# Kernel tuning notes

Hardware: AMD Instinct MI355X
Metric: run time of the kernel (lower is better)

The kernel has to match this reference:

```python
import jax, jax.numpy as jnp
import numpy as np

EPS = 1e-5
NUM_HEAD = 8
HEAD_DIM = 64
SCALE = HEAD_DIM ** -0.5


def setup_inputs() -> dict:
    key = jax.random.key(0)
    ks = jax.random.split(key, 3)
    b, n, dim = 4, 2048, 512
    inner = NUM_HEAD * HEAD_DIM  # 512
    x = jax.random.normal(ks[0], (b, n, dim), dtype=jnp.float32)
    ln_w = jnp.ones((dim,), jnp.float32)
    ln_b = jnp.zeros((dim,), jnp.float32)
    qkv_w = jax.random.normal(ks[1], (3 * inner, dim), jnp.float32) * (dim ** -0.5)
    qkv_b = jnp.zeros((3 * inner,), jnp.float32)
    out_w = jax.random.normal(ks[2], (dim, inner), jnp.float32) * (inner ** -0.5)
    out_b = jnp.zeros((dim,), jnp.float32)
    return {"x": x, "ln_w": ln_w, "ln_b": ln_b, "qkv_w": qkv_w,
            "qkv_b": qkv_b, "out_w": out_w, "out_b": out_b}


def reference(x, ln_w, ln_b, qkv_w, qkv_b, out_w, out_b):
    b, n, dim = x.shape
    # Pre-norm LayerNorm
    mu = jnp.mean(x, axis=-1, keepdims=True)
    var = jnp.mean(jnp.square(x - mu), axis=-1, keepdims=True)
    xn = (x - mu) * jax.lax.rsqrt(var + EPS) * ln_w + ln_b
    # QKV projection (torch Linear: y = x @ W.T + b)
    qkv = xn @ qkv_w.T + qkv_b  # [b, n, 3*inner]
    q, k, v = jnp.split(qkv, 3, axis=-1)
    def heads(t):  # [b, n, inner] -> [b, h, n, d]
        return t.reshape(b, n, NUM_HEAD, HEAD_DIM).transpose(0, 2, 1, 3)
    q, k, v = heads(q), heads(k), heads(v)
    # Naive full attention (materializes [b, h, n, n])
    dots = jnp.einsum('bhqd,bhkd->bhqk', q, k) * SCALE
    attn = jax.nn.softmax(dots, axis=-1)
    o = jnp.einsum('bhqk,bhkd->bhqd', attn, v)
    o = o.transpose(0, 2, 1, 3).reshape(b, n, NUM_HEAD * HEAD_DIM)
    return o @ out_w.T + out_b
```

## Files before the change

kernel.cpp:

```cpp
#include <hip/hip_runtime.h>

typedef __attribute__((ext_vector_type(8))) short bf16x8;
typedef __attribute__((ext_vector_type(4))) float floatx4;
typedef __attribute__((ext_vector_type(16))) float floatx16;
typedef __attribute__((ext_vector_type(4))) unsigned int uintx4;

#define B_    4
#define N_    2048
#define DIM_  512
#define NH_   8
#define HD_   64
#define SCALE_ 0.125f
#define SL2E_ (0.125f * 1.44269504f)

__device__ __forceinline__ unsigned short f32_to_bf16(float f) {
    return (unsigned short)((__float_as_uint(f) + 0x8000u) >> 16);
}

__device__ __forceinline__ float bf16_to_f32(unsigned short u) {
    return __uint_as_float(((unsigned int)u) << 16);
}

__device__ __forceinline__ floatx4 mfma16(bf16x8 a, bf16x8 b, floatx4 c) {
    return __builtin_amdgcn_mfma_f32_16x16x32_bf16(a, b, c, 0, 0, 0);
}

__device__ __forceinline__ floatx16 mfma32(bf16x8 a, bf16x8 b, floatx16 c) {
    return __builtin_amdgcn_mfma_f32_32x32x16_bf16(a, b, c, 0, 0, 0);
}

__device__ __forceinline__ floatx4 fzero4() {
    floatx4 z = {0.f, 0.f, 0.f, 0.f};
    return z;
}

__device__ __forceinline__ floatx16 fzero16() {
    floatx16 z;
#pragma unroll
    for (int i = 0; i < 16; i++) z[i] = 0.f;
    return z;
}

__device__ __forceinline__ unsigned int cvt_pk_bf16(float lo, float hi) {
    unsigned int r;
    asm("v_cvt_pk_bf16_f32 %0, %1, %2" : "=v"(r) : "v"(lo), "v"(hi));
    return r;
}

__device__ __forceinline__ void async16(const unsigned short* g, unsigned short* l) {
    __builtin_amdgcn_global_load_lds((const __attribute__((address_space(1))) void*)g,
                                     (__attribute__((address_space(3))) void*)l,
                                     16, 0, 0);
}

__global__ __launch_bounds__(256) void ln_kernel(const float* __restrict__ x,
                                                 const float* __restrict__ w,
                                                 const float* __restrict__ b,
                                                 unsigned short* __restrict__ xn) {
    int wv = threadIdx.x >> 6;
    int lane = threadIdx.x & 63;
    int row = blockIdx.x * 4 + wv;
    const float4* xr = (const float4*)(x + (size_t)row * DIM_);
    float4 v0 = xr[lane * 2];
    float4 v1 = xr[lane * 2 + 1];
    float s  = (v0.x + v0.y + v0.z + v0.w) + (v1.x + v1.y + v1.z + v1.w);
    float sq = v0.x*v0.x + v0.y*v0.y + v0.z*v0.z + v0.w*v0.w +
               v1.x*v1.x + v1.y*v1.y + v1.z*v1.z + v1.w*v1.w;
#pragma unroll
    for (int off = 1; off < 64; off <<= 1) {
        s  += __shfl_xor(s, off, 64);
        sq += __shfl_xor(sq, off, 64);
    }
    float mu   = s * (1.f / DIM_);
    float var  = sq * (1.f / DIM_) - mu * mu;
    float rstd = rsqrtf(var + 1e-5f);
    float4 w0 = ((const float4*)w)[lane * 2];
    float4 w1 = ((const float4*)w)[lane * 2 + 1];
    float4 b0 = ((const float4*)b)[lane * 2];
    float4 b1 = ((const float4*)b)[lane * 2 + 1];
    float y[8];
    y[0] = (v0.x - mu) * rstd * w0.x + b0.x;
    y[1] = (v0.y - mu) * rstd * w0.y + b0.y;
    y[2] = (v0.z - mu) * rstd * w0.z + b0.z;
    y[3] = (v0.w - mu) * rstd * w0.w + b0.w;
    y[4] = (v1.x - mu) * rstd * w1.x + b1.x;
    y[5] = (v1.y - mu) * rstd * w1.y + b1.y;
    y[6] = (v1.z - mu) * rstd * w1.z + b1.z;
    y[7] = (v1.w - mu) * rstd * w1.w + b1.w;
    uint4 pk;
    pk.x = (unsigned int)f32_to_bf16(y[0]) | ((unsigned int)f32_to_bf16(y[1]) << 16);
    pk.y = (unsigned int)f32_to_bf16(y[2]) | ((unsigned int)f32_to_bf16(y[3]) << 16);
    pk.z = (unsigned int)f32_to_bf16(y[4]) | ((unsigned int)f32_to_bf16(y[5]) << 16);
    pk.w = (unsigned int)f32_to_bf16(y[6]) | ((unsigned int)f32_to_bf16(y[7]) << 16);
    ((uint4*)(xn + (size_t)row * DIM_))[lane] = pk;
}

__global__ __launch_bounds__(256) void cvt_kernel(const float* __restrict__ srcA, int na,
                                                  const float* __restrict__ srcB, int nb,
                                                  unsigned short* __restrict__ dstA,
                                                  unsigned short* __restrict__ dstB) {
    int idx = blockIdx.x * 256 + threadIdx.x;
    if (idx < na)            dstA[idx] = f32_to_bf16(srcA[idx]);
    else if (idx < na + nb)  dstB[idx - na] = f32_to_bf16(srcB[idx - na]);
}

#define GEMM_CORE512(A_, B_ptr, am0, bn0)                                           \
    __shared__ unsigned short Alds[2][128][32];                                     \
    __shared__ unsigned short Blds[2][128][32];                                     \
    int tid = threadIdx.x, lane = tid & 63, wid = tid >> 6;                         \
    int l15 = lane & 15, quad = lane >> 4;                                          \
    int wmloc = (wid >> 1) * 32, wnloc = (wid & 1) * 64;                            \
    int sr = lane >> 2;                                                             \
    int sc = (lane & 3) * 8;                                                        \
    int srow0 = 16 * wid;                                                           \
    floatx4 acc[2][4];                                                              \
    _Pragma("unroll")                                                               \
    for (int i = 0; i < 2; i++)                                                     \
        _Pragma("unroll")                                                           \
        for (int j = 0; j < 4; j++) acc[i][j] = fzero4();                           \
    int buf = 0;                                                                    \
    async16(A_ + (size_t)(am0 + srow0 + sr) * DIM_ + sc, &Alds[0][srow0][0]);       \
    async16(B_ptr + (size_t)(bn0 + srow0 + sr) * DIM_ + sc, &Blds[0][srow0][0]);    \
    __syncthreads();                                                                \
    for (int t = 0; t < 16; t++) {                                                  \
        if (t < 15) {                                                               \
            int k0 = (t + 1) * 32;                                                  \
            async16(A_ + (size_t)(am0 + srow0 + sr) * DIM_ + k0 + sc,               \
                    &Alds[buf ^ 1][srow0][0]);                                      \
            async16(B_ptr + (size_t)(bn0 + srow0 + sr) * DIM_ + k0 + sc,            \
                    &Blds[buf ^ 1][srow0][0]);                                      \
        }                                                                           \
        bf16x8 av[2], bv[4];                                                        \
        _Pragma("unroll")                                                           \
        for (int i = 0; i < 2; i++)                                                 \
            av[i] = *(const bf16x8*)(&Alds[buf][wmloc + 16 * i + l15][quad * 8]);   \
        _Pragma("unroll")                                                           \
        for (int j = 0; j < 4; j++)                                                 \
            bv[j] = *(const bf16x8*)(&Blds[buf][wnloc + 16 * j + l15][quad * 8]);   \
        _Pragma("unroll")                                                           \
        for (int i = 0; i < 2; i++)                                                 \
            _Pragma("unroll")                                                       \
            for (int j = 0; j < 4; j++)                                             \
                acc[i][j] = mfma16(av[i], bv[j], acc[i][j]);                        \
        __syncthreads();                                                            \
        buf ^= 1;                                                                   \
    }

__global__ __launch_bounds__(512, 4) void qkv_gemm(const unsigned short* __restrict__ A,
                                                   const unsigned short* __restrict__ Bw,
                                                   const float* __restrict__ bias,
                                                   unsigned short* __restrict__ Qh,
                                                   unsigned short* __restrict__ Kh,
                                                   unsigned short* __restrict__ Vt) {
    int am0 = blockIdx.x * 128, bn0 = blockIdx.y * 128;
    GEMM_CORE512(A, Bw, am0, bn0)

    if (bn0 >= 1024) {
        unsigned short* sc_ = &Alds[0][0][0] + wid * (16 * 40);
        int m0 = am0 + wmloc;
        int bidx = m0 >> 11;
        int t0 = m0 & 2047;
#pragma unroll
        for (int j = 0; j < 4; j++) {
            float bias_n = bias[bn0 + wnloc + 16 * j + l15];
#pragma unroll
            for (int i = 0; i < 2; i++)
#pragma unroll
                for (int r = 0; r < 4; r++)
                    sc_[l15 * 40 + 16 * i + quad * 4 + r] =
                        f32_to_bf16(acc[i][j][r] + bias_n);
            int nr = lane >> 2;
            int rem = (bn0 - 1024) + wnloc + 16 * j + nr;
            int head = rem >> 6, d = rem & 63;
            bf16x8 vv = *(const bf16x8*)(sc_ + nr * 40 + (lane & 3) * 8);
            *(bf16x8*)(Vt + ((size_t)(bidx * NH_ + head) * HD_ + d) * N_ +
                       t0 + (lane & 3) * 8) = vv;
        }
    } else {
#pragma unroll
        for (int i = 0; i < 2; i++) {
#pragma unroll
            for (int j = 0; j < 4; j++) {
                int n = bn0 + wnloc + 16 * j + l15;
                float bias_n = bias[n];
                int which = n >> 9;
                int rem = n & 511;
                int head = rem >> 6;
                int d = rem & 63;
#pragma unroll
                for (int r = 0; r < 4; r++) {
                    int m = am0 + wmloc + 16 * i + quad * 4 + r;
                    int b = m >> 11;
                    int t = m & 2047;
                    float val = acc[i][j][r] + bias_n;
                    if (which == 0) {
                        Qh[((size_t)(b * NH_ + head) * N_ + t) * HD_ + d] =
                            f32_to_bf16(val * SL2E_);
                    } else {
                        Kh[((size_t)(b * NH_ + head) * N_ + t) * HD_ + d] =
                            f32_to_bf16(val);
                    }
                }
            }
        }
    }
}

__global__ __launch_bounds__(256, 4) void out_gemm_fused(const unsigned short* __restrict__ Opart,
                                                         const float* __restrict__ lpart,
                                                         const unsigned short* __restrict__ Bw,
                                                         const float* __restrict__ bias,
                                                         float* __restrict__ out) {
    __shared__ unsigned short Alds[2][64][36];
    __shared__ unsigned short Blds[2][128][32];
    int tid = threadIdx.x, lane = tid & 63, wid = tid >> 6;
    int l15 = lane & 15, quad = lane >> 4;
    int wmloc = (wid >> 1) * 32, wnloc = (wid & 1) * 64;
    int am0 = blockIdx.x * 64, bn0 = blockIdx.y * 128;

    int arow = tid >> 2;
    int ac8 = (tid & 3) * 8;
    int token = am0 + arow;
    int bb = token >> 11;
    const size_t LSTR = (size_t)B_ * NH_ * N_;
    const size_t OSTR = (size_t)B_ * N_ * DIM_;
    const unsigned short* arow0 = Opart + (size_t)token * DIM_;
    const unsigned short* arow1 = arow0 + OSTR;

    int sr = lane >> 2;
    int sc = (lane & 3) * 8;

    floatx4 acc[2][4];
#pragma unroll
    for (int i = 0; i < 2; i++)
#pragma unroll
        for (int j = 0; j < 4; j++) acc[i][j] = fzero4();

#define STAGE_A(BUF, T)                                                         \
    {                                                                           \
        int k0 = (T) * 32;                                                      \
        int head = k0 >> 6;                                                     \
        size_t li = (size_t)(bb * NH_ + head) * N_ + (token & 2047);            \
        float l1 = lpart[li];                                                   \
        float l2 = lpart[LSTR + li];                                            \
        float inv = 1.f / (l1 + l2);                                            \
        float w1 = l1 * inv, w2 = l2 * inv;                                     \
        bf16x8 o0 = *(const bf16x8*)(arow0 + k0 + ac8);                         \
        bf16x8 o1 = *(const bf16x8*)(arow1 + k0 + ac8);                         \
        bf16x8 pk;                                                              \
        _Pragma("unroll")                                                       \
        for (int e = 0; e < 8; e++)                                             \
            pk[e] = (short)f32_to_bf16(                                         \
                w1 * bf16_to_f32((unsigned short)o0[e]) +                       \
                w2 * bf16_to_f32((unsigned short)o1[e]));                       \
        *(bf16x8*)(&Alds[BUF][arow][ac8]) = pk;                                 \
    }

#define STAGE_B(BUF, T)                                                         \
    {                                                                           \
        int k0 = (T) * 32;                                                      \
        _Pragma("unroll")                                                       \
        for (int i = 0; i < 2; i++) {                                           \
            int r0 = 32 * wid + 16 * i;                                         \
            async16(Bw + (size_t)(bn0 + r0 + sr) * DIM_ + k0 + sc,              \
                    &Blds[BUF][r0][0]);                                         \
        }                                                                       \
    }

    STAGE_B(0, 0)
    STAGE_A(0, 0)
    __syncthreads();
    int buf = 0;
    for (int t = 0; t < 16; t++) {
        if (t < 15) {
            STAGE_B(buf ^ 1, t + 1)
            STAGE_A(buf ^ 1, t + 1)
        }
        bf16x8 av[2], bv[4];
#pragma unroll
        for (int i = 0; i < 2; i++)
            av[i] = *(const bf16x8*)(&Alds[buf][wmloc + 16 * i + l15][quad * 8]);
#pragma unroll
        for (int j = 0; j < 4; j++)
            bv[j] = *(const bf16x8*)(&Blds[buf][wnloc + 16 * j + l15][quad * 8]);
#pragma unroll
        for (int i = 0; i < 2; i++)
#pragma unroll
            for (int j = 0; j < 4; j++)
                acc[i][j] = mfma16(av[i], bv[j], acc[i][j]);
        __syncthreads();
        buf ^= 1;
    }
#undef STAGE_A
#undef STAGE_B

#pragma unroll
    for (int i = 0; i < 2; i++) {
#pragma unroll
        for (int j = 0; j < 4; j++) {
            int n = bn0 + wnloc + 16 * j + l15;
            float bias_n = bias[n];
#pragma unroll
            for (int r = 0; r < 4; r++) {
                int m = am0 + wmloc + 16 * i + quad * 4 + r;
                out[(size_t)m * DIM_ + n] = acc[i][j][r] + bias_n;
            }
        }
    }
}

__global__ __launch_bounds__(256, 4) void attn_kernel(const unsigned short* __restrict__ Qh,
                                                      const unsigned short* __restrict__ Kh,
                                                      const unsigned short* __restrict__ Vtg,
                                                      unsigned short* __restrict__ Opart,
                                                      float* __restrict__ lpart) {
    int bh = blockIdx.y;
    int b = bh >> 3, head = bh & 7;
    int qt = blockIdx.x;
    int split = blockIdx.z;
    int kv0 = split << 10;
    int tid = threadIdx.x, lane = tid & 63, w = tid >> 6;
    int l31 = lane & 31, hi = lane >> 5;
    int xr = l31 & 7;

    const unsigned short* Qp = Qh + (size_t)bh * N_ * HD_;
    const unsigned short* Kg = Kh + (size_t)bh * N_ * HD_;
    const unsigned short* Vg = Vtg + (size_t)bh * HD_ * N_;

    int q0 = qt * 128 + w * 32;

    bf16x8 aQ[4];
    {
        const unsigned short* qrow = Qp + (size_t)(q0 + l31) * HD_ + hi * 8;
#pragma unroll
        for (int t = 0; t < 4; t++)
            aQ[t] = *(const bf16x8*)(qrow + 16 * t);
    }

    __shared__ unsigned short KV[2][2][64][64];

    int srow = lane >> 3;
    int scol = ((lane & 7) ^ srow) * 8;

    const char* ptc[4];
#pragma unroll
    for (int t = 0; t < 4; t++)
        ptc[t] = (const char*)&KV[0][0][l31][(((2 * t + hi) ^ xr) * 8)];

    const unsigned short* kSrc = Kg + (size_t)(kv0 + 16 * w + srow) * HD_ + scol;
    const unsigned short* vSrc = Vg + (size_t)(16 * w + srow) * N_ + kv0 + scol;

#define STAGE_KV(BUF, IT)                                                       \
    {                                                                           \
        _Pragma("unroll")                                                       \
        for (int i = 0; i < 2; i++) {                                           \
            int r0 = 16 * w + 8 * i;                                            \
            async16(kSrc + (size_t)(IT) * 64 * HD_ + i * 8 * HD_,               \
                    &KV[BUF][0][r0][0]);                                        \
            async16(vSrc + (size_t)(IT) * 64 + i * 8 * N_,                      \
                    &KV[BUF][1][r0][0]);                                        \
        }                                                                       \
    }

    floatx16 of[2];
    of[0] = fzero16();
    of[1] = fzero16();
    floatx16 lacc = fzero16();

    const short onebf = (short)0x3F80;
    bf16x8 onesB = {onebf, onebf, onebf, onebf, onebf, onebf, onebf, onebf};

#define COMPUTE(BUF)                                                            \
    {                                                                           \
        bf16x8 pa[4];                                                           \
        _Pragma("unroll")                                                       \
        for (int tau = 0; tau < 2; tau++) {                                     \
            bf16x8 kf[4];                                                       \
            _Pragma("unroll")                                                   \
            for (int t = 0; t < 4; t++)                                         \
                kf[t] = *(const bf16x8*)(ptc[t] + (BUF) * 16384 + tau * 4096);  \
            floatx16 acc = fzero16();                                           \
            __builtin_amdgcn_s_setprio(1);                                      \
            _Pragma("unroll")                                                   \
            for (int t = 0; t < 4; t++)                                         \
                acc = mfma32(kf[t], aQ[t], acc);                                \
            __builtin_amdgcn_s_setprio(0);                                      \
            float p[16];                                                        \
            _Pragma("unroll")                                                   \
            for (int r = 0; r < 16; r++)                                        \
                p[r] = __builtin_amdgcn_exp2f(acc[r]);                          \
            unsigned int a0 = cvt_pk_bf16(p[0], p[1]);                          \
            unsigned int b0 = cvt_pk_bf16(p[4], p[5]);                          \
            unsigned int a1 = cvt_pk_bf16(p[2], p[3]);                          \
            unsigned int b1 = cvt_pk_bf16(p[6], p[7]);                          \
            unsigned int a2 = cvt_pk_bf16(p[8], p[9]);                          \
            unsigned int b2 = cvt_pk_bf16(p[12], p[13]);                        \
            unsigned int a3 = cvt_pk_bf16(p[10], p[11]);                        \
            unsigned int b3 = cvt_pk_bf16(p[14], p[15]);                        \
            asm("v_permlane32_swap_b32 %0, %1" : "+v"(a0), "+v"(b0));           \
            asm("v_permlane32_swap_b32 %0, %1" : "+v"(a1), "+v"(b1));           \
            asm("v_permlane32_swap_b32 %0, %1" : "+v"(a2), "+v"(b2));           \
            asm("v_permlane32_swap_b32 %0, %1" : "+v"(a3), "+v"(b3));           \
            uintx4 f0 = {a0, a1, b0, b1};                                       \
            uintx4 f1 = {a2, a3, b2, b3};                                       \
            pa[2 * tau]     = __builtin_bit_cast(bf16x8, f0);                   \
            pa[2 * tau + 1] = __builtin_bit_cast(bf16x8, f1);                   \
        }                                                                       \
        __builtin_amdgcn_s_setprio(1);                                          \
        _Pragma("unroll")                                                       \
        for (int s = 0; s < 4; s++) {                                           \
            _Pragma("unroll")                                                   \
            for (int dt = 0; dt < 2; dt++) {                                    \
                bf16x8 vf = *(const bf16x8*)(ptc[s] + (BUF) * 16384 + 8192 +    \
                                             dt * 4096);                        \
                of[dt] = mfma32(pa[s], vf, of[dt]);                             \
            }                                                                   \
            lacc = mfma32(pa[s], onesB, lacc);                                  \
        }                                                                       \
        __builtin_amdgcn_s_setprio(0);                                          \
    }

    STAGE_KV(0, 0)
    __syncthreads();

    for (int it2 = 0; it2 < 8; it2++) {
        int it = it2 * 2;
        STAGE_KV(1, it + 1)
        COMPUTE(0)
        __syncthreads();
        if (it2 < 7) STAGE_KV(0, it + 2)
        COMPUTE(1)
        __syncthreads();
    }
#undef STAGE_KV
#undef COMPUTE

    unsigned short* Od = Opart + (size_t)split * B_ * N_ * DIM_;
#pragma unroll
    for (int r = 0; r < 16; r++) {
        int qr = (r & 3) + 8 * (r >> 2) + 4 * hi;
        float inv = __builtin_amdgcn_rcpf(lacc[r]);
        int token = q0 + qr;
        size_t base = ((size_t)b * N_ + token) * DIM_ + (size_t)head * HD_;
#pragma unroll
        for (int dt = 0; dt < 2; dt++)
            Od[base + 32 * dt + l31] = f32_to_bf16(of[dt][r] * inv);
    }
    if (l31 == 0) {
#pragma unroll
        for (int r = 0; r < 16; r++) {
            int qr = (r & 3) + 8 * (r >> 2) + 4 * hi;
            lpart[(size_t)split * B_ * NH_ * N_ + (size_t)bh * N_ + q0 + qr] =
                lacc[r];
        }
    }
}

extern "C" void kernel_launch(void* const* d_in, const int* in_sizes, int n_in,
                              void* d_out, int out_size, void* d_ws, size_t ws_size,
                              hipStream_t stream) {
    const float* x     = (const float*)d_in[0];
    const float* ln_w  = (const float*)d_in[1];
    const float* ln_b  = (const float*)d_in[2];
    const float* qkv_w = (const float*)d_in[3];
    const float* qkv_b = (const float*)d_in[4];
    const float* out_w = (const float*)d_in[5];
    const float* out_b = (const float*)d_in[6];
    float* out = (float*)d_out;

    char* ws = (char*)d_ws;
    const size_t TOK = (size_t)B_ * N_;
    unsigned short* xn    = (unsigned short*)ws;  ws += TOK * DIM_ * 2;
    unsigned short* wq_bf = (unsigned short*)ws;  ws += (size_t)3 * DIM_ * DIM_ * 2;
    unsigned short* wo_bf = (unsigned short*)ws;  ws += (size_t)DIM_ * DIM_ * 2;
    unsigned short* Qh    = (unsigned short*)ws;  ws += TOK * DIM_ * 2;
    unsigned short* Kh    = (unsigned short*)ws;  ws += TOK * DIM_ * 2;
    unsigned short* Vt    = (unsigned short*)ws;  ws += TOK * DIM_ * 2;
    unsigned short* Opart = (unsigned short*)ws;  ws += (size_t)2 * TOK * DIM_ * 2;
    float*          lpart = (float*)ws;           ws += (size_t)2 * B_ * NH_ * N_ * 4;

    const int NW = 3 * DIM_ * DIM_;
    const int NO = DIM_ * DIM_;

    ln_kernel<<<TOK / 4, 256, 0, stream>>>(x, ln_w, ln_b, xn);
    cvt_kernel<<<(NW + NO + 255) / 256, 256, 0, stream>>>(qkv_w, NW, out_w, NO, wq_bf, wo_bf);
    qkv_gemm<<<dim3(TOK / 128, (3 * DIM_) / 128), 512, 0, stream>>>(xn, wq_bf, qkv_b, Qh, Kh, Vt);
    attn_kernel<<<dim3(N_ / 128, B_ * NH_, 2), 256, 0, stream>>>(Qh, Kh, Vt, Opart, lpart);
    out_gemm_fused<<<dim3(TOK / 64, DIM_ / 128), 256, 0, stream>>>(Opart, lpart, wo_bf, out_b, out);
}
```

Before: 161.2 us.

## Fuse layernorm with weight conversion and stage QKV epilogue through LDS

Merges the layernorm and fp32-to-bf16 weight conversion kernels into one launch, with the conversion now vectorised to eight elements per thread. The Q/K epilogue of the QKV GEMM writes into shared memory first, then stores contiguous 16-byte rows instead of scattered 2-byte writes. It also raises the GEMM occupancy hint to 6 and seeds the first attention MFMA with a zero constant. The aim is fewer launches and better-coalesced global stores, at the cost of reusing the A tile buffer as scratch and possible register pressure from the occupancy change.

Measured after the change: 156.5 us (median of 2 runs). 2.9% less time.

```diff
diff --git a/kernel.cpp b/kernel.cpp
--- a/kernel.cpp
+++ b/kernel.cpp
@@ -53,55 +53,67 @@
                                      16, 0, 0);
 }
 
-__global__ __launch_bounds__(256) void ln_kernel(const float* __restrict__ x,
-                                                 const float* __restrict__ w,
-                                                 const float* __restrict__ b,
-                                                 unsigned short* __restrict__ xn) {
-    int wv = threadIdx.x >> 6;
-    int lane = threadIdx.x & 63;
-    int row = blockIdx.x * 4 + wv;
-    const float4* xr = (const float4*)(x + (size_t)row * DIM_);
-    float4 v0 = xr[lane * 2];
-    float4 v1 = xr[lane * 2 + 1];
-    float s  = (v0.x + v0.y + v0.z + v0.w) + (v1.x + v1.y + v1.z + v1.w);
-    float sq = v0.x*v0.x + v0.y*v0.y + v0.z*v0.z + v0.w*v0.w +
-               v1.x*v1.x + v1.y*v1.y + v1.z*v1.z + v1.w*v1.w;
-#pragma unroll
-    for (int off = 1; off < 64; off <<= 1) {
-        s  += __shfl_xor(s, off, 64);
-        sq += __shfl_xor(sq, off, 64);
-    }
-    float mu   = s * (1.f / DIM_);
-    float var  = sq * (1.f / DIM_) - mu * mu;
-    float rstd = rsqrtf(var + 1e-5f);
-    float4 w0 = ((const float4*)w)[lane * 2];
-    float4 w1 = ((const float4*)w)[lane * 2 + 1];
-    float4 b0 = ((const float4*)b)[lane * 2];
-    float4 b1 = ((const float4*)b)[lane * 2 + 1];
-    float y[8];
-    y[0] = (v0.x - mu) * rstd * w0.x + b0.x;
-    y[1] = (v0.y - mu) * rstd * w0.y + b0.y;
-    y[2] = (v0.z - mu) * rstd * w0.z + b0.z;
-    y[3] = (v0.w - mu) * rstd * w0.w + b0.w;
-    y[4] = (v1.x - mu) * rstd * w1.x + b1.x;
-    y[5] = (v1.y - mu) * rstd * w1.y + b1.y;
-    y[6] = (v1.z - mu) * rstd * w1.z + b1.z;
-    y[7] = (v1.w - mu) * rstd * w1.w + b1.w;
-    uint4 pk;
-    pk.x = (unsigned int)f32_to_bf16(y[0]) | ((unsigned int)f32_to_bf16(y[1]) << 16);
-    pk.y = (unsigned int)f32_to_bf16(y[2]) | ((unsigned int)f32_to_bf16(y[3]) << 16);
-    pk.z = (unsigned int)f32_to_bf16(y[4]) | ((unsigned int)f32_to_bf16(y[5]) << 16);
-    pk.w = (unsigned int)f32_to_bf16(y[6]) | ((unsigned int)f32_to_bf16(y[7]) << 16);
-    ((uint4*)(xn + (size_t)row * DIM_))[lane] = pk;
-}
-
-__global__ __launch_bounds__(256) void cvt_kernel(const float* __restrict__ srcA, int na,
-                                                  const float* __restrict__ srcB, int nb,
-                                                  unsigned short* __restrict__ dstA,
-                                                  unsigned short* __restrict__ dstB) {
-    int idx = blockIdx.x * 256 + threadIdx.x;
-    if (idx < na)            dstA[idx] = f32_to_bf16(srcA[idx]);
-    else if (idx < na + nb)  dstB[idx - na] = f32_to_bf16(srcB[idx - na]);
+__global__ __launch_bounds__(256) void ln_cvt_kernel(const float* __restrict__ x,
+                                                     const float* __restrict__ w,
+                                                     const float* __restrict__ b,
+                                                     unsigned short* __restrict__ xn,
+                                                     const float* __restrict__ srcA,
+                                                     const float* __restrict__ srcB,
+                                                     unsigned short* __restrict__ dstA,
+                                                     unsigned short* __restrict__ dstB) {
+    const int NWQ = 3 * DIM_ * DIM_;
+    if (blockIdx.x < 2048) {
+        int wv = threadIdx.x >> 6;
+        int lane = threadIdx.x & 63;
+        int row = blockIdx.x * 4 + wv;
+        const float4* xr = (const float4*)(x + (size_t)row * DIM_);
+        float4 v0 = xr[lane * 2];
+        float4 v1 = xr[lane * 2 + 1];
+        float s  = (v0.x + v0.y + v0.z + v0.w) + (v1.x + v1.y + v1.z + v1.w);
+        float sq = v0.x*v0.x + v0.y*v0.y + v0.z*v0.z + v0.w*v0.w +
+                   v1.x*v1.x + v1.y*v1.y + v1.z*v1.z + v1.w*v1.w;
+#pragma unroll
+        for (int off = 1; off < 64; off <<= 1) {
+            s  += __shfl_xor(s, off, 64);
+            sq += __shfl_xor(sq, off, 64);
+        }
+        float mu   = s * (1.f / DIM_);
+        float var  = sq * (1.f / DIM_) - mu * mu;
+        float rstd = rsqrtf(var + 1e-5f);
+        float4 w0 = ((const float4*)w)[lane * 2];
+        float4 w1 = ((const float4*)w)[lane * 2 + 1];
+        float4 b0 = ((const float4*)b)[lane * 2];
+        float4 b1 = ((const float4*)b)[lane * 2 + 1];
+        float y[8];
+        y[0] = (v0.x - mu) * rstd * w0.x + b0.x;
+        y[1] = (v0.y - mu) * rstd * w0.y + b0.y;
+        y[2] = (v0.z - mu) * rstd * w0.z + b0.z;
+        y[3] = (v0.w - mu) * rstd * w0.w + b0.w;
+        y[4] = (v1.x - mu) * rstd * w1.x + b1.x;
+        y[5] = (v1.y - mu) * rstd * w1.y + b1.y;
+        y[6] = (v1.z - mu) * rstd * w1.z + b1.z;
+        y[7] = (v1.w - mu) * rstd * w1.w + b1.w;
+        uint4 pk;
+        pk.x = (unsigned int)f32_to_bf16(y[0]) | ((unsigned int)f32_to_bf16(y[1]) << 16);
+        pk.y = (unsigned int)f32_to_bf16(y[2]) | ((unsigned int)f32_to_bf16(y[3]) << 16);
+        pk.z = (unsigned int)f32_to_bf16(y[4]) | ((unsigned int)f32_to_bf16(y[5]) << 16);
+        pk.w = (unsigned int)f32_to_bf16(y[6]) | ((unsigned int)f32_to_bf16(y[7]) << 16);
+        ((uint4*)(xn + (size_t)row * DIM_))[lane] = pk;
+    } else {
+        int e0 = ((blockIdx.x - 2048) * 256 + threadIdx.x) * 8;
+        const float* src;
+        unsigned short* dst;
+        if (e0 < NWQ) { src = srcA + e0; dst = dstA + e0; }
+        else          { src = srcB + (e0 - NWQ); dst = dstB + (e0 - NWQ); }
+        float4 u0 = ((const float4*)src)[0];
+        float4 u1 = ((const float4*)src)[1];
+        uint4 pk;
+        pk.x = (unsigned int)f32_to_bf16(u0.x) | ((unsigned int)f32_to_bf16(u0.y) << 16);
+        pk.y = (unsigned int)f32_to_bf16(u0.z) | ((unsigned int)f32_to_bf16(u0.w) << 16);
+        pk.z = (unsigned int)f32_to_bf16(u1.x) | ((unsigned int)f32_to_bf16(u1.y) << 16);
+        pk.w = (unsigned int)f32_to_bf16(u1.z) | ((unsigned int)f32_to_bf16(u1.w) << 16);
+        *(uint4*)dst = pk;
+    }
 }
 
 #define GEMM_CORE512(A_, B_ptr, am0, bn0)                                           \
@@ -146,7 +158,7 @@
         buf ^= 1;                                                                   \
     }
 
-__global__ __launch_bounds__(512, 4) void qkv_gemm(const unsigned short* __restrict__ A,
+__global__ __launch_bounds__(512, 6) void qkv_gemm(const unsigned short* __restrict__ A,
                                                    const unsigned short* __restrict__ Bw,
                                                    const float* __restrict__ bias,
                                                    unsigned short* __restrict__ Qh,
@@ -177,30 +189,31 @@
                        t0 + (lane & 3) * 8) = vv;
         }
     } else {
+        unsigned short* sc2 = &Alds[0][0][0] + wid * 1024;
+        int n0 = bn0 + wnloc;
+        int which = n0 >> 9;
+        int head = (n0 & 511) >> 6;
+        unsigned short* dstBase = (which == 0) ? Qh : Kh;
+        float mul = (which == 0) ? SL2E_ : 1.f;
 #pragma unroll
         for (int i = 0; i < 2; i++) {
 #pragma unroll
             for (int j = 0; j < 4; j++) {
-                int n = bn0 + wnloc + 16 * j + l15;
-                float bias_n = bias[n];
-                int which = n >> 9;
-                int rem = n & 511;
-                int head = rem >> 6;
-                int d = rem & 63;
-#pragma unroll
-                for (int r = 0; r < 4; r++) {
-                    int m = am0 + wmloc + 16 * i + quad * 4 + r;
-                    int b = m >> 11;
-                    int t = m & 2047;
-                    float val = acc[i][j][r] + bias_n;
-                    if (which == 0) {
-                        Qh[((size_t)(b * NH_ + head) * N_ + t) * HD_ + d] =
-                            f32_to_bf16(val * SL2E_);
-                    } else {
-                        Kh[((size_t)(b * NH_ + head) * N_ + t) * HD_ + d] =
-                            f32_to_bf16(val);
-                    }
-                }
+                float bias_n = bias[n0 + 16 * j + l15];
+#pragma unroll
+                for (int r = 0; r < 4; r++)
+                    sc2[(quad * 4 + r) * 64 + 16 * j + l15] =
+                        f32_to_bf16((acc[i][j][r] + bias_n) * mul);
+            }
+            asm volatile("s_waitcnt lgkmcnt(0)" ::: "memory");
+#pragma unroll
+            for (int h = 0; h < 2; h++) {
+                int tl = 8 * h + (lane >> 3);
+                int m = am0 + wmloc + 16 * i + tl;
+                int bb2 = m >> 11, tt = m & 2047;
+                bf16x8 row = *(const bf16x8*)(sc2 + tl * 64 + (lane & 7) * 8);
+                *(bf16x8*)(dstBase + ((size_t)(bb2 * NH_ + head) * N_ + tt) * HD_ +
+                           (lane & 7) * 8) = row;
             }
         }
     }
@@ -366,6 +379,7 @@
     of[0] = fzero16();
     of[1] = fzero16();
     floatx16 lacc = fzero16();
+    const floatx16 z16 = fzero16();
 
     const short onebf = (short)0x3F80;
     bf16x8 onesB = {onebf, onebf, onebf, onebf, onebf, onebf, onebf, onebf};
@@ -379,11 +393,11 @@
             _Pragma("unroll")                                                   \
             for (int t = 0; t < 4; t++)                                         \
                 kf[t] = *(const bf16x8*)(ptc[t] + (BUF) * 16384 + tau * 4096);  \
-            floatx16 acc = fzero16();                                           \
             __builtin_amdgcn_s_setprio(1);                                      \
-            _Pragma("unroll")                                                   \
-            for (int t = 0; t < 4; t++)                                         \
-                acc = mfma32(kf[t], aQ[t], acc);                                \
+            floatx16 acc = mfma32(kf[0], aQ[0], z16);                           \
+            acc = mfma32(kf[1], aQ[1], acc);                                    \
+            acc = mfma32(kf[2], aQ[2], acc);                                    \
+            acc = mfma32(kf[3], aQ[3], acc);                                    \
             __builtin_amdgcn_s_setprio(0);                                      \
             float p[16];                                                        \
             _Pragma("unroll")                                                   \
@@ -479,11 +493,8 @@
     unsigned short* Opart = (unsigned short*)ws;  ws += (size_t)2 * TOK * DIM_ * 2;
     float*          lpart = (float*)ws;           ws += (size_t)2 * B_ * NH_ * N_ * 4;
 
-    const int NW = 3 * DIM_ * DIM_;
-    const int NO = DIM_ * DIM_;
-
-    ln_kernel<<<TOK / 4, 256, 0, stream>>>(x, ln_w, ln_b, xn);
-    cvt_kernel<<<(NW + NO + 255) / 256, 256, 0, stream>>>(qkv_w, NW, out_w, NO, wq_bf, wo_bf);
+    ln_cvt_kernel<<<2048 + 512, 256, 0, stream>>>(x, ln_w, ln_b, xn,
+                                                  qkv_w, out_w, wq_bf, wo_bf);
     qkv_gemm<<<dim3(TOK / 128, (3 * DIM_) / 128), 512, 0, stream>>>(xn, wq_bf, qkv_b, Qh, Kh, Vt);
     attn_kernel<<<dim3(N_ / 128, B_ * NH_, 2), 256, 0, stream>>>(Qh, Kh, Vt, Opart, lpart);
     out_gemm_fused<<<dim3(TOK / 64, DIM_ / 128), 256, 0, stream>>>(Opart, lpart, wo_bf, out_b, out);
```
